# Performance work log

Hardware: AMD Instinct MI355X
Metric: run time of the kernel (lower is better)

## Reference

```python
import jax, jax.numpy as jnp
import numpy as np

DIM = 512
HEADS = 8
DH = DIM // HEADS          # 64
M = DIM // 2               # 256 landmarks
PINV_ITERS = 6
KERNEL = 33                # residual_conv_kernel (lucidrains default)
SCALE = DH ** -0.5
LN_EPS = 1e-5


def setup_inputs() -> dict:
    key = jax.random.key(0)
    ks = jax.random.split(key, 6)
    b, n = 4, 4096
    x = jax.random.normal(ks[0], (b, n, DIM), jnp.float32)
    ln_w = jnp.ones((DIM,), jnp.float32)
    ln_b = jnp.zeros((DIM,), jnp.float32)
    w_qkv = jax.random.normal(ks[1], (DIM, 3 * DIM), jnp.float32) / np.float32(np.sqrt(DIM))
    w_out = jax.random.normal(ks[2], (DIM, DIM), jnp.float32) / np.float32(np.sqrt(DIM))
    b_out = jnp.zeros((DIM,), jnp.float32)
    # depthwise Conv2d(heads, heads, (33,1), groups=heads, bias=False): OIHW = (8,1,33,1)
    conv_w = jax.random.normal(ks[3], (HEADS, 1, KERNEL, 1), jnp.float32) / np.float32(np.sqrt(KERNEL))
    # admin_torch.as_module(8): residual x*omega + f(x), omega learnable scalar init sqrt(8)
    omega = jnp.asarray(np.sqrt(8.0), jnp.float32)
    return dict(x=x, ln_w=ln_w, ln_b=ln_b, w_qkv=w_qkv, w_out=w_out,
                b_out=b_out, conv_w=conv_w, omega=omega)


def _layernorm(x, w, b):
    mu = x.mean(-1, keepdims=True)
    var = x.var(-1, keepdims=True)
    return (x - mu) * jax.lax.rsqrt(var + LN_EPS) * w + b


def _moore_penrose_pinv(x, iters):
    # Newton-Schulz iteration, exactly as lucidrains nystrom-attention
    abs_x = jnp.abs(x)
    col = abs_x.sum(-1)
    row = abs_x.sum(-2)
    z = jnp.swapaxes(x, -1, -2) / (jnp.max(col) * jnp.max(row))
    I = jnp.eye(x.shape[-1], dtype=x.dtype)
    for _ in range(iters):
        xz = x @ z
        z = 0.25 * z @ (13. * I - xz @ (15. * I - xz @ (7. * I - xz)))
    return z


def reference(x, ln_w, ln_b, w_qkv, w_out, b_out, conv_w, omega):
    b, n, _ = x.shape
    nx = _layernorm(x, ln_w, ln_b)
    qkv = nx @ w_qkv                                # [b, n, 3*dim]
    q, k, v = jnp.split(qkv, 3, axis=-1)
    to_heads = lambda t: t.reshape(b, n, HEADS, DH).transpose(0, 2, 1, 3)  # bhnd
    q = to_heads(q) * SCALE
    k = to_heads(k)
    v = to_heads(v)
    l = n // M                                      # tokens per landmark group
    q_l = q.reshape(b, HEADS, M, l, DH).mean(3)     # [b,h,m,d]
    k_l = k.reshape(b, HEADS, M, l, DH).mean(3)
    sim1 = jnp.einsum('bhid,bhjd->bhij', q, k_l)    # [b,h,n,m]
    sim2 = jnp.einsum('bhid,bhjd->bhij', q_l, k_l)  # [b,h,m,m]
    sim3 = jnp.einsum('bhid,bhjd->bhij', q_l, k)    # [b,h,m,n]
    a1 = jax.nn.softmax(sim1, -1)
    a2 = jax.nn.softmax(sim2, -1)
    a3 = jax.nn.softmax(sim3, -1)
    a2_inv = _moore_penrose_pinv(a2, PINV_ITERS)
    out = (a1 @ a2_inv) @ (a3 @ v)                  # [b,h,n,d]
    # residual depthwise conv along the sequence dim of v
    res = jax.lax.conv_general_dilated(
        v, conv_w, window_strides=(1, 1),
        padding=((KERNEL // 2, KERNEL // 2), (0, 0)),
        dimension_numbers=('NCHW', 'OIHW', 'NCHW'),
        feature_group_count=HEADS)
    out = out + res
    out = out.transpose(0, 2, 1, 3).reshape(b, n, HEADS * DH)
    out = out @ w_out + b_out                       # to_out (dropout is eval no-op)
    return x * omega + out                          # admin residual
```

## Files before the change

### kernel.cpp

```cpp
#include <hip/hip_runtime.h>
#include <math.h>

#define B_    4
#define N_    4096
#define DIM_  512
#define H_    8
#define DH_   64
#define M_    256
#define LGRP  16
#define BH_   (B_*H_)
#define SCALE_ 0.125f
#define LN_EPS_ 1e-5f

#define SZ_QKVH (B_*H_*N_*DH_)
#define SZ_LM   (BH_*M_*DH_)
#define SZ_MM   (BH_*M_*M_)

typedef unsigned short ushort_t;
typedef __attribute__((ext_vector_type(8))) short bfrag8;
typedef __attribute__((ext_vector_type(4))) float fvec4;

__device__ __forceinline__ ushort_t f2b(float f) {
    unsigned u = __float_as_uint(f);
    unsigned r = (u + 0x7fffu + ((u >> 16) & 1u)) >> 16;
    return (ushort_t)r;
}
__device__ __forceinline__ float b2f(ushort_t s) {
    return __uint_as_float(((unsigned)s) << 16);
}

__global__ __launch_bounds__(256) void ln_kernel(const float* __restrict__ x,
                                                 const float* __restrict__ w,
                                                 const float* __restrict__ bb,
                                                 ushort_t* __restrict__ nxb) {
    int row = blockIdx.x;
    int t = threadIdx.x;
    const float* xr = x + (size_t)row * DIM_;
    float v0 = xr[t], v1 = xr[t + 256];
    float s = v0 + v1, sq = v0 * v0 + v1 * v1;
    __shared__ float ls[4], lq[4];
    for (int off = 32; off > 0; off >>= 1) {
        s  += __shfl_down(s, off);
        sq += __shfl_down(sq, off);
    }
    int wid = t >> 6, lid = t & 63;
    if (lid == 0) { ls[wid] = s; lq[wid] = sq; }
    __syncthreads();
    if (t == 0) {
        float S = 0, Q = 0;
        for (int i = 0; i < 4; i++) { S += ls[i]; Q += lq[i]; }
        ls[0] = S; lq[0] = Q;
    }
    __syncthreads();
    float mean = ls[0] * (1.f / DIM_);
    float var  = lq[0] * (1.f / DIM_) - mean * mean;
    float rs = rsqrtf(var + LN_EPS_);
    ushort_t* o = nxb + (size_t)row * DIM_;
    o[t]       = f2b((v0 - mean) * rs * w[t]       + bb[t]);
    o[t + 256] = f2b((v1 - mean) * rs * w[t + 256] + bb[t + 256]);
}

__global__ __launch_bounds__(256) void tcast(const float* __restrict__ in,
                                             ushort_t* __restrict__ outT,
                                             int R, int C) {
    __shared__ float tile[32][33];
    int c0 = blockIdx.x * 32, r0 = blockIdx.y * 32;
    int t = threadIdx.x;
    #pragma unroll
    for (int u = 0; u < 4; u++) {
        int lin = t + 256 * u;
        int r = lin >> 5, c = lin & 31;
        tile[r][c] = in[(size_t)(r0 + r) * C + c0 + c];
    }
    __syncthreads();
    #pragma unroll
    for (int u = 0; u < 4; u++) {
        int lin = t + 256 * u;
        int cc = lin >> 5, rr = lin & 31;
        outT[(size_t)(c0 + cc) * R + r0 + rr] = f2b(tile[rr][cc]);
    }
}

template<int EPI>
__global__ __launch_bounds__(256) void gemm_bt128(const ushort_t* __restrict__ A,
                                                  const ushort_t* __restrict__ BT,
                                                  ushort_t* __restrict__ qb,
                                                  ushort_t* __restrict__ kb,
                                                  ushort_t* __restrict__ vb,
                                                  const float* __restrict__ x,
                                                  const float* __restrict__ bo,
                                                  const float* __restrict__ omega,
                                                  float* __restrict__ out) {
    const int K = 512;
    __shared__ __align__(16) ushort_t smem[2 * 128 * 72];
    ushort_t (*As)[72] = (ushort_t(*)[72])smem;
    ushort_t (*Bs)[72] = (ushort_t(*)[72])(smem + 128 * 72);
    int t = threadIdx.x;
    int lin = blockIdx.x + blockIdx.y * gridDim.x;
    int nwg = gridDim.x * gridDim.y;
    int wg  = (lin & 7) * (nwg >> 3) + (lin >> 3);
    int n0 = (wg % gridDim.x) * 128, m0 = (wg / gridDim.x) * 128;
    int w = t >> 6, lane = t & 63;
    int wr = (w >> 1) * 64, wc = (w & 1) * 64;
    int l15 = lane & 15, quad = lane >> 4, kq = quad * 8;
    fvec4 acc[4][4] = {};
    int rbase = t >> 3, c8 = (t & 7) * 8;

    for (int kc = 0; kc < K; kc += 64) {
        #pragma unroll
        for (int u = 0; u < 4; u++) {
            int rr = rbase + 32 * u;
            const ushort_t* ga;
            if (EPI == 0) {
                ga = A + (size_t)(m0 + rr) * K + kc + c8;
            } else {
                int grow = m0 + rr; int b_ = grow >> 12, nn = grow & 4095;
                int col = kc + c8; int hd = col >> 6, dd = col & 63;
                ga = A + (((size_t)(b_ * H_ + hd) * N_ + nn) << 6) + dd;
            }
            *(float4*)&As[rr][c8] = *(const float4*)ga;
            *(float4*)&Bs[rr][c8] = *(const float4*)(BT + (size_t)(n0 + rr) * K + kc + c8);
        }
        __syncthreads();
        #pragma unroll
        for (int ks = 0; ks < 64; ks += 32) {
            bfrag8 a[4], b[4];
            #pragma unroll
            for (int r = 0; r < 4; r++) a[r] = *(bfrag8*)&As[wr + r * 16 + l15][ks + kq];
            #pragma unroll
            for (int c = 0; c < 4; c++) b[c] = *(bfrag8*)&Bs[wc + c * 16 + l15][ks + kq];
            #pragma unroll
            for (int r = 0; r < 4; r++)
                #pragma unroll
                for (int c = 0; c < 4; c++)
                    acc[r][c] = __builtin_amdgcn_mfma_f32_16x16x32_bf16(a[r], b[c], acc[r][c], 0, 0, 0);
        }
        __syncthreads();
    }

    if (EPI == 0) {
        int sec = n0 >> 9;
        float mul = (sec == 0) ? SCALE_ : 1.0f;
        ushort_t (*Ct)[132] = (ushort_t(*)[132])smem;
        #pragma unroll
        for (int r = 0; r < 4; r++) {
            #pragma unroll
            for (int reg = 0; reg < 4; reg++) {
                int lr = wr + r * 16 + quad * 4 + reg;
                #pragma unroll
                for (int c = 0; c < 4; c++) {
                    int lc = wc + c * 16 + l15;
                    Ct[lr][lc] = f2b(acc[r][c][reg] * mul);
                }
            }
        }
        __syncthreads();
        int row = t & 127, half = t >> 7;
        int grow = m0 + row; int b_ = grow >> 12, nn = grow & 4095;
        int head = ((n0 & 511) >> 6) + half;
        ushort_t* dstbuf = (sec == 0) ? qb : ((sec == 1) ? kb : vb);
        ushort_t* dp = dstbuf + (((size_t)(b_ * H_ + head) * N_ + nn) << 6);
        #pragma unroll
        for (int i = 0; i < 8; i++)
            *(uint4*)(dp + i * 8) = *(uint4*)&Ct[row][half * 64 + i * 8];
    } else {
        float om = omega[0];
        #pragma unroll
        for (int r = 0; r < 4; r++) {
            #pragma unroll
            for (int reg = 0; reg < 4; reg++) {
                int grow = m0 + wr + r * 16 + quad * 4 + reg;
                #pragma unroll
                for (int c = 0; c < 4; c++) {
                    int gcol = n0 + wc + c * 16 + l15;
                    size_t o = (size_t)grow * DIM_ + gcol;
                    out[o] = om * x[o] + bo[gcol] + acc[r][c][reg];
                }
            }
        }
    }
}

__global__ __launch_bounds__(256) void landmark_kernel(const ushort_t* __restrict__ q,
                                                       const ushort_t* __restrict__ k,
                                                       ushort_t* __restrict__ ql,
                                                       ushort_t* __restrict__ kl) {
    int idx = blockIdx.x * 256 + threadIdx.x;
    const ushort_t* src = blockIdx.y ? k : q;
    ushort_t* dst = blockIdx.y ? kl : ql;
    int d8 = (idx & 7) * 8;
    int m = (idx >> 3) & 255;
    int bh = idx >> 11;
    const ushort_t* p = src + (((size_t)bh * N_) + m * LGRP) * DH_ + d8;
    float s[8] = {};
    #pragma unroll
    for (int j = 0; j < LGRP; j++) {
        union { uint4 u4; ushort_t sv[8]; } val;
        val.u4 = *(const uint4*)(p + (size_t)j * DH_);
        #pragma unroll
        for (int e = 0; e < 8; e++) s[e] += b2f(val.sv[e]);
    }
    union { uint4 u4; ushort_t sv[8]; } o;
    #pragma unroll
    for (int e = 0; e < 8; e++) o.sv[e] = f2b(s[e] * (1.f / LGRP));
    *(uint4*)(dst + ((size_t)bh * M_ + m) * DH_ + d8) = o.u4;
}

__global__ __launch_bounds__(256) void sim2_softmax(const ushort_t* __restrict__ ql,
                                                    const ushort_t* __restrict__ kl,
                                                    float* __restrict__ a2,
                                                    ushort_t* __restrict__ a2b) {
    int i = blockIdx.x, bh = blockIdx.y, j = threadIdx.x;
    __shared__ float qrow[64];
    __shared__ float red[256];
    if (j < 64) qrow[j] = b2f(ql[((size_t)bh * M_ + i) * DH_ + j]);
    __syncthreads();
    const ushort_t* kr = kl + ((size_t)bh * M_ + j) * DH_;
    float s = 0;
    #pragma unroll
    for (int d = 0; d < 64; d++) s += qrow[d] * b2f(kr[d]);
    red[j] = s; __syncthreads();
    for (int off = 128; off > 0; off >>= 1) {
        if (j < off) red[j] = fmaxf(red[j], red[j + off]);
        __syncthreads();
    }
    float mx = red[0]; __syncthreads();
    float p = __expf(s - mx);
    red[j] = p; __syncthreads();
    for (int off = 128; off > 0; off >>= 1) {
        if (j < off) red[j] += red[j + off];
        __syncthreads();
    }
    float res = p / red[0];
    size_t o = ((size_t)bh * M_ + i) * M_ + j;
    a2[o] = res;
    a2b[o] = f2b(res);
}

__global__ void zero2(unsigned* p) { if (threadIdx.x < 2) p[threadIdx.x] = 0u; }

__global__ __launch_bounds__(256) void colpart(const float* __restrict__ a2,
                                               float* __restrict__ cs2) {
    int bh = blockIdx.x, s = blockIdx.y, t = threadIdx.x;
    const float* A = a2 + ((size_t)bh << 16) + (size_t)s * 32 * M_;
    float cs = 0.f;
    #pragma unroll
    for (int i = 0; i < 32; i++) cs += A[(size_t)i * M_ + t];
    cs2[((size_t)s * BH_ + bh) * M_ + t] = cs;
}

__global__ __launch_bounds__(256) void colmax(const float* __restrict__ cs2, unsigned* red) {
    int bh = blockIdx.x, t = threadIdx.x;
    float v = 0.f;
    #pragma unroll
    for (int s = 0; s < 8; s++) v += cs2[((size_t)s * BH_ + bh) * M_ + t];
    __shared__ float lr[256];
    lr[t] = v; __syncthreads();
    for (int off = 128; off > 0; off >>= 1) {
        if (t < off) lr[t] = fmaxf(lr[t], lr[t + off]);
        __syncthreads();
    }
    if (t == 0) atomicMax(red, __float_as_uint(lr[0]));
}

__global__ __launch_bounds__(256) void pinv_init2(const float* __restrict__ a2,
                                                  const unsigned* __restrict__ red,
                                                  ushort_t* __restrict__ zA,
                                                  ushort_t* __restrict__ zAT) {
    __shared__ float tile[32][33];
    int bt = blockIdx.z; int j0 = blockIdx.x * 32, i0 = blockIdx.y * 32;
    float invd = 1.f / __uint_as_float(red[0]);
    const float* Ab = a2 + ((size_t)bt << 16);
    size_t bo = (size_t)bt << 16;
    int t = threadIdx.x;
    #pragma unroll
    for (int u = 0; u < 4; u++) {
        int lin = t + 256 * u; int r = lin >> 5, c = lin & 31;
        float vv = Ab[(size_t)(i0 + r) * M_ + j0 + c] * invd;
        tile[r][c] = vv;
        zAT[bo + (size_t)(i0 + r) * M_ + j0 + c] = f2b(vv);
    }
    __syncthreads();
    #pragma unroll
    for (int u = 0; u < 4; u++) {
        int lin = t + 256 * u; int cc = lin >> 5, rr = lin & 31;
        zA[bo + (size_t)(j0 + cc) * M_ + i0 + rr] = f2b(tile[rr][cc]);
    }
}

__global__ __launch_bounds__(256) void gemm_pinv(const ushort_t* __restrict__ A,
                                                 const ushort_t* __restrict__ BT,
                                                 ushort_t* __restrict__ outN,
                                                 ushort_t* __restrict__ outT,
                                                 ushort_t* __restrict__ outT1,
                                                 float* __restrict__ outF,
                                                 float coefI, float scale) {
    __shared__ __align__(16) ushort_t As[64][72];
    __shared__ __align__(16) ushort_t Bs[64][72];
    int t = threadIdx.x; int bt = blockIdx.z;
    const ushort_t* Ab = A + ((size_t)bt << 16);
    const ushort_t* Bb = BT + ((size_t)bt << 16);
    int n0 = blockIdx.x * 64, m0 = blockIdx.y * 64;
    int w = t >> 6, lane = t & 63;
    int wr = (w >> 1) * 32, wc = (w & 1) * 32;
    int l15 = lane & 15, quad = lane >> 4, kq = quad * 8;
    fvec4 acc[2][2] = {};
    int rbase = t >> 3, c8 = (t & 7) * 8;

    for (int kc = 0; kc < M_; kc += 64) {
        #pragma unroll
        for (int u = 0; u < 2; u++) {
            int rr = rbase + 32 * u;
            *(float4*)&As[rr][c8] = *(const float4*)(Ab + (size_t)(m0 + rr) * M_ + kc + c8);
            *(float4*)&Bs[rr][c8] = *(const float4*)(Bb + (size_t)(n0 + rr) * M_ + kc + c8);
        }
        __syncthreads();
        #pragma unroll
        for (int ks = 0; ks < 64; ks += 32) {
            bfrag8 a[2], b[2];
            #pragma unroll
            for (int r = 0; r < 2; r++) a[r] = *(bfrag8*)&As[wr + r * 16 + l15][ks + kq];
            #pragma unroll
            for (int c = 0; c < 2; c++) b[c] = *(bfrag8*)&Bs[wc + c * 16 + l15][ks + kq];
            #pragma unroll
            for (int r = 0; r < 2; r++)
                #pragma unroll
                for (int c = 0; c < 2; c++)
                    acc[r][c] = __builtin_amdgcn_mfma_f32_16x16x32_bf16(a[r], b[c], acc[r][c], 0, 0, 0);
        }
        __syncthreads();
    }

    size_t bto = (size_t)bt << 16;
    if (outN || outF) {
        #pragma unroll
        for (int r = 0; r < 2; r++) {
            #pragma unroll
            for (int reg = 0; reg < 4; reg++) {
                int grow = m0 + wr + r * 16 + quad * 4 + reg;
                #pragma unroll
                for (int c = 0; c < 2; c++) {
                    int gcol = n0 + wc + c * 16 + l15;
                    float cv = scale * acc[r][c][reg] + (grow == gcol ? coefI : 0.f);
                    if (outN) outN[bto + (size_t)grow * M_ + gcol] = f2b(cv);
                    if (outF) outF[bto + (size_t)grow * M_ + gcol] = cv;
                }
            }
        }
    }
    if (outT || outT1) {
        ushort_t (*Ct)[65] = (ushort_t(*)[65])&As[0][0];
        #pragma unroll
        for (int r = 0; r < 2; r++) {
            #pragma unroll
            for (int reg = 0; reg < 4; reg++) {
                int lr = wr + r * 16 + quad * 4 + reg;
                #pragma unroll
                for (int c = 0; c < 2; c++) {
                    int lc = wc + c * 16 + l15;
                    float cv = scale * acc[r][c][reg] + ((m0 + lr) == (n0 + lc) ? coefI : 0.f);
                    Ct[lr][lc] = f2b(cv);
                }
            }
        }
        __syncthreads();
        int j = t & 63, quarter = t >> 6, i0 = quarter * 16;
        #pragma unroll
        for (int vq = 0; vq < 2; vq++) {
            union { uint4 u4; ushort_t s[8]; } o1, o2;
            #pragma unroll
            for (int e = 0; e < 8; e++) {
                int il = i0 + vq * 8 + e;
                ushort_t bv = Ct[il][j];
                o1.s[e] = bv;
                o2.s[e] = f2b(((m0 + il) == (n0 + j) ? 7.f : 0.f) - b2f(bv));
            }
            size_t dst = bto + (size_t)(n0 + j) * M_ + m0 + i0 + vq * 8;
            if (outT)  *(uint4*)&outT[dst]  = o1.u4;
            if (outT1) *(uint4*)&outT1[dst] = o2.u4;
        }
    }
}

template<int NCH, int TRANSV>
__global__ __launch_bounds__(256) void flash_mfma(const ushort_t* __restrict__ Q,
                                                  const ushort_t* __restrict__ K,
                                                  const ushort_t* __restrict__ V,
                                                  ushort_t* __restrict__ Obf,
                                                  float* __restrict__ Opart,
                                                  float* __restrict__ lout,
                                                  int nq, int nk) {
    int bh = blockIdx.y;
    int nqt = nq >> 6;
    int qt = blockIdx.x % nqt;
    int ch = blockIdx.x / nqt;
    int q0 = qt * 64;
    int chunk = nk / NCH;
    int j0 = ch * chunk, j1 = j0 + chunk;

    __shared__ __align__(16) ushort_t qs[64][72];
    __shared__ __align__(16) ushort_t ks[64][72];
    __shared__ __align__(16) ushort_t vts[64][72];
    __shared__ __align__(16) ushort_t pb[64][72];

    int t = threadIdx.x;
    int w = t >> 6, lane = t & 63;
    int l15 = lane & 15, quad = lane >> 4, kq = quad * 8;
    int wrow = w * 16;

    const ushort_t* Qb = Q + ((size_t)bh * nq + q0) * DH_;
    #pragma unroll
    for (int u = 0; u < 2; u++) {
        int lin = t + 256 * u;
        int r = lin >> 3, cc = (lin & 7) * 8;
        *(uint4*)&qs[r][cc] = *(const uint4*)(Qb + r * DH_ + cc);
    }

    fvec4 Oacc[4];
    #pragma unroll
    for (int nt = 0; nt < 4; nt++)
        #pragma unroll
        for (int reg = 0; reg < 4; reg++) Oacc[nt][reg] = 0.f;
    float l_[4] = {0.f, 0.f, 0.f, 0.f};

    const ushort_t* VTbase = V + (size_t)bh * DH_ * nk;
    for (int j = j0; j < j1; j += 64) {
        const ushort_t* Kb = K + ((size_t)bh * nk + j) * DH_;
        const ushort_t* Vb = V + ((size_t)bh * nk + j) * DH_;
        #pragma unroll
        for (int u = 0; u < 2; u++) {
            int lin = t + 256 * u;
            int r = lin >> 3, cc = (lin & 7) * 8;
            *(uint4*)&ks[r][cc] = *(const uint4*)(Kb + r * DH_ + cc);
            if (TRANSV == 0) {
                *(uint4*)&vts[r][cc] = *(const uint4*)(VTbase + (size_t)r * nk + j + cc);
            } else {
                union { uint4 u4; ushort_t s[8]; } vv;
                vv.u4 = *(const uint4*)(Vb + r * DH_ + cc);
                #pragma unroll
                for (int m = 0; m < 8; m++) vts[cc + m][r] = vv.s[m];
            }
        }
        __syncthreads();

        fvec4 S[4];
        #pragma unroll
        for (int ct = 0; ct < 4; ct++)
            #pragma unroll
            for (int reg = 0; reg < 4; reg++) S[ct][reg] = 0.f;
        bfrag8 aq0 = *(bfrag8*)&qs[wrow + l15][kq];
        bfrag8 aq1 = *(bfrag8*)&qs[wrow + l15][32 + kq];
        #pragma unroll
        for (int ct = 0; ct < 4; ct++) {
            bfrag8 b0 = *(bfrag8*)&ks[ct * 16 + l15][kq];
            bfrag8 b1 = *(bfrag8*)&ks[ct * 16 + l15][32 + kq];
            S[ct] = __builtin_amdgcn_mfma_f32_16x16x32_bf16(aq0, b0, S[ct], 0, 0, 0);
            S[ct] = __builtin_amdgcn_mfma_f32_16x16x32_bf16(aq1, b1, S[ct], 0, 0, 0);
        }

        float ps[4] = {0.f, 0.f, 0.f, 0.f};
        #pragma unroll
        for (int ct = 0; ct < 4; ct++) {
            #pragma unroll
            for (int reg = 0; reg < 4; reg++) {
                float pv = __expf(S[ct][reg]);
                ps[reg] += pv;
                pb[wrow + quad * 4 + reg][ct * 16 + l15] = f2b(pv);
            }
        }
        #pragma unroll
        for (int reg = 0; reg < 4; reg++) {
            float s = ps[reg];
            s += __shfl_xor(s, 1);
            s += __shfl_xor(s, 2);
            s += __shfl_xor(s, 4);
            s += __shfl_xor(s, 8);
            l_[reg] += s;
        }

        bfrag8 ap0 = *(bfrag8*)&pb[wrow + l15][kq];
        bfrag8 ap1 = *(bfrag8*)&pb[wrow + l15][32 + kq];
        #pragma unroll
        for (int nt = 0; nt < 4; nt++) {
            bfrag8 b0 = *(bfrag8*)&vts[nt * 16 + l15][kq];
            bfrag8 b1 = *(bfrag8*)&vts[nt * 16 + l15][32 + kq];
            Oacc[nt] = __builtin_amdgcn_mfma_f32_16x16x32_bf16(ap0, b0, Oacc[nt], 0, 0, 0);
            Oacc[nt] = __builtin_amdgcn_mfma_f32_16x16x32_bf16(ap1, b1, Oacc[nt], 0, 0, 0);
        }
        __syncthreads();
    }

    if (NCH == 1) {
        #pragma unroll
        for (int reg = 0; reg < 4; reg++) {
            float inv = 1.f / l_[reg];
            #pragma unroll
            for (int nt = 0; nt < 4; nt++)
                qs[wrow + quad * 4 + reg][nt * 16 + l15] = f2b(Oacc[nt][reg] * inv);
        }
        __syncthreads();
        ushort_t* Ob = Obf + ((size_t)bh * nq + q0) * DH_;
        #pragma unroll
        for (int u = 0; u < 2; u++) {
            int lin = t + 256 * u;
            int r = lin >> 3, i = (lin & 7) * 8;
            *(uint4*)(Ob + (size_t)r * DH_ + i) = *(uint4*)&qs[r][i];
        }
    } else {
        size_t rows_per_ch = (size_t)BH_ * nq;
        #pragma unroll
        for (int reg = 0; reg < 4; reg++) {
            size_t rowg = (size_t)bh * nq + q0 + wrow + quad * 4 + reg;
            #pragma unroll
            for (int nt = 0; nt < 4; nt++)
                Opart[((size_t)ch * rows_per_ch + rowg) * DH_ + nt * 16 + l15] = Oacc[nt][reg];
            if (l15 == 0)
                lout[(size_t)ch * rows_per_ch + rowg] = l_[reg];
        }
    }
}

__global__ __launch_bounds__(256) void flash_combine(const float* __restrict__ apart,
                                                     const float* __restrict__ lpart,
                                                     ushort_t* __restrict__ a3vb) {
    int idx = blockIdx.x * 256 + threadIdx.x;
    int d = idx & 63; int row = idx >> 6;
    const int R = BH_ * M_;
    float l = lpart[row] + lpart[row + R] + lpart[row + 2 * R] + lpart[row + 3 * R];
    size_t e = (size_t)row * DH_ + d;
    const size_t CH = (size_t)R * DH_;
    float o = apart[e] + apart[e + CH] + apart[e + 2 * CH] + apart[e + 3 * CH];
    a3vb[e] = f2b(o / l);
}

__global__ __launch_bounds__(256) void wm_mfma(const ushort_t* __restrict__ Z,
                                               const ushort_t* __restrict__ A3V,
                                               ushort_t* __restrict__ WmT) {
    __shared__ __align__(16) ushort_t As[64][72];
    __shared__ __align__(16) ushort_t Bs[64][72];
    int bh = blockIdx.y;
    int i0 = blockIdx.x * 64;
    const ushort_t* Zb = Z + ((size_t)bh << 16);
    const ushort_t* Ab = A3V + ((size_t)bh << 14);
    int t = threadIdx.x;
    int w = t >> 6, lane = t & 63;
    int wr = (w >> 1) * 32, wc = (w & 1) * 32;
    int l15 = lane & 15, quad = lane >> 4, kq = quad * 8;
    fvec4 acc[2][2] = {};
    int rbase = t >> 3, c8 = (t & 7) * 8;

    for (int kc = 0; kc < M_; kc += 64) {
        #pragma unroll
        for (int u = 0; u < 2; u++) {
            int rr = rbase + 32 * u;
            *(float4*)&Bs[rr][c8] = *(const float4*)(Zb + (size_t)(i0 + rr) * M_ + kc + c8);
            union { uint4 u4; ushort_t s[8]; } av;
            av.u4 = *(const uint4*)(Ab + (size_t)(kc + rr) * DH_ + c8);
            #pragma unroll
            for (int m = 0; m < 8; m++) As[c8 + m][rr] = av.s[m];
        }
        __syncthreads();
        #pragma unroll
        for (int ks = 0; ks < 64; ks += 32) {
            bfrag8 a[2], b[2];
            #pragma unroll
            for (int r = 0; r < 2; r++) a[r] = *(bfrag8*)&As[wr + r * 16 + l15][ks + kq];
            #pragma unroll
            for (int c = 0; c < 2; c++) b[c] = *(bfrag8*)&Bs[wc + c * 16 + l15][ks + kq];
            #pragma unroll
            for (int r = 0; r < 2; r++)
                #pragma unroll
                for (int c = 0; c < 2; c++)
                    acc[r][c] = __builtin_amdgcn_mfma_f32_16x16x32_bf16(a[r], b[c], acc[r][c], 0, 0, 0);
        }
        __syncthreads();
    }
    #pragma unroll
    for (int r = 0; r < 2; r++) {
        #pragma unroll
        for (int reg = 0; reg < 4; reg++) {
            int drow = wr + r * 16 + quad * 4 + reg;
            ushort_t* dp = WmT + ((size_t)bh * DH_ + drow) * M_;
            #pragma unroll
            for (int c = 0; c < 2; c++)
                dp[i0 + wc + c * 16 + l15] = f2b(acc[r][c][reg]);
        }
    }
}

__global__ __launch_bounds__(256) void conv_kernel(const ushort_t* __restrict__ V,
                                                   const float* __restrict__ cw,
                                                   const ushort_t* __restrict__ ctxb,
                                                   ushort_t* __restrict__ outb) {
    int bh = blockIdx.y;
    int h = bh & 7;
    int i0 = blockIdx.x * 64;
    __shared__ float vb[96][64];
    __shared__ float wloc[33];
    int t = threadIdx.x;
    if (t < 33) wloc[t] = cw[h * 33 + t];
    #pragma unroll
    for (int u = 0; u < 3; u++) {
        int lin = t + 256 * u;
        int r = lin >> 3, cc = (lin & 7) * 8;
        int gi = i0 - 16 + r;
        union { uint4 u4; ushort_t s[8]; } val;
        if (gi >= 0 && gi < N_)
            val.u4 = *(const uint4*)(V + ((size_t)bh * N_ + gi) * DH_ + cc);
        else
            val.u4 = make_uint4(0, 0, 0, 0);
        #pragma unroll
        for (int m = 0; m < 8; m++) vb[r][cc + m] = b2f(val.s[m]);
    }
    __syncthreads();
    int d = t & 63, rb = t >> 6;
    for (int u = 0; u < 16; u++) {
        int r = rb * 16 + u;
        float s = 0.f;
        #pragma unroll
        for (int kk = 0; kk < 33; kk++) s += wloc[kk] * vb[r + kk][d];
        size_t o = ((size_t)bh * N_ + i0 + r) * DH_ + d;
        outb[o] = f2b(b2f(ctxb[o]) + s);
    }
}

extern "C" void kernel_launch(void* const* d_in, const int* in_sizes, int n_in,
                              void* d_out, int out_size, void* d_ws, size_t ws_size,
                              hipStream_t stream) {
    const float* x      = (const float*)d_in[0];
    const float* ln_w   = (const float*)d_in[1];
    const float* ln_b   = (const float*)d_in[2];
    const float* w_qkv  = (const float*)d_in[3];
    const float* w_out  = (const float*)d_in[4];
    const float* b_out  = (const float*)d_in[5];
    const float* conv_w = (const float*)d_in[6];
    const float* omega  = (const float*)d_in[7];
    float* out = (float*)d_out;

    float* fp = (float*)d_ws;
    float* a2    = fp;              fp += SZ_MM;
    float* apart = fp;              fp += SZ_QKVH / 4;
    float* lpart = fp;              fp += 4 * BH_ * M_;
    float* cs2   = fp;              fp += 8 * BH_ * M_;
    ushort_t* us = (ushort_t*)fp;
    ushort_t* wqkvT = us;           us += DIM_ * 3 * DIM_;
    ushort_t* woT   = us;           us += DIM_ * DIM_;
    ushort_t* a2b   = us;           us += SZ_MM;
    ushort_t* zA    = us;           us += SZ_MM;
    ushort_t* zAT   = us;           us += SZ_MM;
    ushort_t* zB    = us;           us += SZ_MM;
    ushort_t* zBT   = us;           us += SZ_MM;
    ushort_t* qb    = us;           us += SZ_QKVH;
    ushort_t* kb    = us;           us += SZ_QKVH;
    ushort_t* vb    = us;           us += SZ_QKVH;
    ushort_t* ctxb  = us;           us += SZ_QKVH;
    ushort_t* outhb = us;           us += SZ_QKVH;
    ushort_t* ql    = us;           us += SZ_LM;
    ushort_t* kl    = us;           us += SZ_LM;
    ushort_t* WmT   = us;           us += SZ_LM;
    ushort_t* a3vb  = us;           us += SZ_LM;
    unsigned* red   = (unsigned*)us;
    ushort_t* nxb = outhb;
    ushort_t* xz  = ctxb;
    ushort_t* t1T = xz  + SZ_MM;
    ushort_t* t2T = t1T + SZ_MM;
    ushort_t* t3T = t2T + SZ_MM;

    ln_kernel<<<B_ * N_, 256, 0, stream>>>(x, ln_w, ln_b, nxb);
    tcast<<<dim3(48, 16), 256, 0, stream>>>(w_qkv, wqkvT, DIM_, 3 * DIM_);
    tcast<<<dim3(16, 16), 256, 0, stream>>>(w_out, woT, DIM_, DIM_);
    gemm_bt128<0><<<dim3(12, 128), 256, 0, stream>>>(nxb, wqkvT, qb, kb, vb,
                                                     nullptr, nullptr, nullptr, nullptr);
    landmark_kernel<<<dim3(256, 2), 256, 0, stream>>>(qb, kb, ql, kl);
    sim2_softmax<<<dim3(M_, BH_), 256, 0, stream>>>(ql, kl, a2, a2b);
    zero2<<<1, 64, 0, stream>>>(red);
    colpart<<<dim3(BH_, 8), 256, 0, stream>>>(a2, cs2);
    colmax<<<BH_, 256, 0, stream>>>(cs2, red);
    pinv_init2<<<dim3(8, 8, 32), 256, 0, stream>>>(a2, red, zA, zAT);

    ushort_t* za = zA;  ushort_t* zaT = zAT;
    ushort_t* zb = zB;  ushort_t* zbT = zBT;
    for (int it = 0; it < 6; it++) {
        gemm_pinv<<<dim3(4, 4, BH_), 256, 0, stream>>>(a2b, zaT, xz, nullptr, t1T, nullptr, 0.f, 1.f);
        gemm_pinv<<<dim3(4, 4, BH_), 256, 0, stream>>>(xz, t1T, nullptr, t2T, nullptr, nullptr, 15.f, -1.f);
        gemm_pinv<<<dim3(4, 4, BH_), 256, 0, stream>>>(xz, t2T, nullptr, t3T, nullptr, nullptr, 13.f, -1.f);
        gemm_pinv<<<dim3(4, 4, BH_), 256, 0, stream>>>(za, t3T, zb, (it < 5) ? zbT : nullptr,
                                                       nullptr, nullptr, 0.f, 0.25f);
        ushort_t* tp;
        tp = za; za = zb; zb = tp;
        tp = zaT; zaT = zbT; zbT = tp;
    }

    flash_mfma<4, 1><<<dim3(16, BH_), 256, 0, stream>>>(ql, kb, vb, nullptr, apart, lpart, M_, N_);
    flash_combine<<<(BH_ * M_ * DH_) / 256, 256, 0, stream>>>(apart, lpart, a3vb);
    wm_mfma<<<dim3(4, BH_), 256, 0, stream>>>(za, a3vb, WmT);
    flash_mfma<1, 0><<<dim3(64, BH_), 256, 0, stream>>>(qb, kl, WmT, ctxb, nullptr, nullptr, N_, M_);
    conv_kernel<<<dim3(N_ / 64, BH_), 256, 0, stream>>>(vb, conv_w, ctxb, outhb);
    gemm_bt128<1><<<dim3(4, 128), 256, 0, stream>>>(outhb, woT, nullptr, nullptr, nullptr,
                                                    x, b_out, omega, out);
}
```

Measured before the change: 523.7 us.

## Double-buffer GEMM tiles via direct global-to-LDS loads and prefetch attention K/V

The QKV/output GEMM and the pinv GEMM now stage tiles with global_load_lds straight into LDS, double-buffering so the next k-tile loads while MFMAs run on the current one. The pinv GEMM also gets a swizzled workgroup-to-tile mapping for locality. The attention kernel prefetches the next K/V block into registers before the current compute. The aim is to hide global load latency. In exchange the LDS row padding is removed, which may cause bank conflicts, and correct synchronisation of asynchronous LDS writes is a risk.

```diff
diff --git a/kernel.cpp b/kernel.cpp
--- a/kernel.cpp
+++ b/kernel.cpp
@@ -27,6 +27,12 @@
 }
 __device__ __forceinline__ float b2f(ushort_t s) {
     return __uint_as_float(((unsigned)s) << 16);
+}
+
+__device__ __forceinline__ void gload16(const ushort_t* g, ushort_t* l) {
+    __builtin_amdgcn_global_load_lds(
+        (const __attribute__((address_space(1))) void*)g,
+        (__attribute__((address_space(3))) void*)l, 16, 0, 0);
 }
 
 __global__ __launch_bounds__(256) void ln_kernel(const float* __restrict__ x,
@@ -92,9 +98,7 @@
                                                   const float* __restrict__ omega,
                                                   float* __restrict__ out) {
     const int K = 512;
-    __shared__ __align__(16) ushort_t smem[2 * 128 * 72];
-    ushort_t (*As)[72] = (ushort_t(*)[72])smem;
-    ushort_t (*Bs)[72] = (ushort_t(*)[72])(smem + 128 * 72);
+    __shared__ __align__(16) ushort_t smem[4 * 128 * 64];
     int t = threadIdx.x;
     int lin = blockIdx.x + blockIdx.y * gridDim.x;
     int nwg = gridDim.x * gridDim.y;
@@ -103,32 +107,42 @@
     int w = t >> 6, lane = t & 63;
     int wr = (w >> 1) * 64, wc = (w & 1) * 64;
     int l15 = lane & 15, quad = lane >> 4, kq = quad * 8;
+    int lrow = lane >> 3, lc8 = (lane & 7) * 8;
     fvec4 acc[4][4] = {};
-    int rbase = t >> 3, c8 = (t & 7) * 8;
-
-    for (int kc = 0; kc < K; kc += 64) {
+
+    auto stage = [&](int buf, int kc) {
+        ushort_t* Ad = smem + buf * 16384;
+        ushort_t* Bd = Ad + 8192;
         #pragma unroll
         for (int u = 0; u < 4; u++) {
-            int rr = rbase + 32 * u;
+            int r0 = (w << 5) + (u << 3);
+            int row = r0 + lrow;
             const ushort_t* ga;
             if (EPI == 0) {
-                ga = A + (size_t)(m0 + rr) * K + kc + c8;
+                ga = A + (size_t)(m0 + row) * K + kc + lc8;
             } else {
-                int grow = m0 + rr; int b_ = grow >> 12, nn = grow & 4095;
-                int col = kc + c8; int hd = col >> 6, dd = col & 63;
-                ga = A + (((size_t)(b_ * H_ + hd) * N_ + nn) << 6) + dd;
+                int grow = m0 + row; int b_ = grow >> 12, nn = grow & 4095;
+                ga = A + (((size_t)(b_ * H_ + (kc >> 6)) * N_ + nn) << 6) + lc8;
             }
-            *(float4*)&As[rr][c8] = *(const float4*)ga;
-            *(float4*)&Bs[rr][c8] = *(const float4*)(BT + (size_t)(n0 + rr) * K + kc + c8);
-        }
-        __syncthreads();
+            gload16(ga, Ad + r0 * 64);
+            gload16(BT + (size_t)(n0 + row) * K + kc + lc8, Bd + r0 * 64);
+        }
+    };
+
+    stage(0, 0);
+    __syncthreads();
+    int cur = 0;
+    for (int kt = 0; kt < 8; ++kt) {
+        if (kt < 7) stage(cur ^ 1, (kt + 1) * 64);
+        const ushort_t* As = smem + cur * 16384;
+        const ushort_t* Bs = As + 8192;
         #pragma unroll
         for (int ks = 0; ks < 64; ks += 32) {
             bfrag8 a[4], b[4];
             #pragma unroll
-            for (int r = 0; r < 4; r++) a[r] = *(bfrag8*)&As[wr + r * 16 + l15][ks + kq];
-            #pragma unroll
-            for (int c = 0; c < 4; c++) b[c] = *(bfrag8*)&Bs[wc + c * 16 + l15][ks + kq];
+            for (int r = 0; r < 4; r++) a[r] = *(bfrag8*)(As + (wr + r * 16 + l15) * 64 + ks + kq);
+            #pragma unroll
+            for (int c = 0; c < 4; c++) b[c] = *(bfrag8*)(Bs + (wc + c * 16 + l15) * 64 + ks + kq);
             #pragma unroll
             for (int r = 0; r < 4; r++)
                 #pragma unroll
@@ -136,6 +150,7 @@
                     acc[r][c] = __builtin_amdgcn_mfma_f32_16x16x32_bf16(a[r], b[c], acc[r][c], 0, 0, 0);
         }
         __syncthreads();
+        cur ^= 1;
     }
 
     if (EPI == 0) {
@@ -295,33 +310,46 @@
                                                  ushort_t* __restrict__ outT1,
                                                  float* __restrict__ outF,
                                                  float coefI, float scale) {
-    __shared__ __align__(16) ushort_t As[64][72];
-    __shared__ __align__(16) ushort_t Bs[64][72];
-    int t = threadIdx.x; int bt = blockIdx.z;
+    __shared__ __align__(16) ushort_t smem[2 * 8192];
+    int t = threadIdx.x;
+    int lin = blockIdx.x + (blockIdx.y << 2) + (blockIdx.z << 4);
+    int wg  = (lin & 7) * 64 + (lin >> 3);
+    int n0 = (wg & 3) * 64, m0 = ((wg >> 2) & 3) * 64;
+    int bt = wg >> 4;
     const ushort_t* Ab = A + ((size_t)bt << 16);
     const ushort_t* Bb = BT + ((size_t)bt << 16);
-    int n0 = blockIdx.x * 64, m0 = blockIdx.y * 64;
     int w = t >> 6, lane = t & 63;
     int wr = (w >> 1) * 32, wc = (w & 1) * 32;
     int l15 = lane & 15, quad = lane >> 4, kq = quad * 8;
+    int lrow = lane >> 3, lc8 = (lane & 7) * 8;
     fvec4 acc[2][2] = {};
-    int rbase = t >> 3, c8 = (t & 7) * 8;
-
-    for (int kc = 0; kc < M_; kc += 64) {
+
+    auto stage = [&](int buf, int kc) {
+        ushort_t* Ad = smem + buf * 8192;
+        ushort_t* Bd = Ad + 4096;
         #pragma unroll
         for (int u = 0; u < 2; u++) {
-            int rr = rbase + 32 * u;
-            *(float4*)&As[rr][c8] = *(const float4*)(Ab + (size_t)(m0 + rr) * M_ + kc + c8);
-            *(float4*)&Bs[rr][c8] = *(const float4*)(Bb + (size_t)(n0 + rr) * M_ + kc + c8);
-        }
-        __syncthreads();
+            int r0 = (w << 4) + (u << 3);
+            int row = r0 + lrow;
+            gload16(Ab + (size_t)(m0 + row) * M_ + kc + lc8, Ad + r0 * 64);
+            gload16(Bb + (size_t)(n0 + row) * M_ + kc + lc8, Bd + r0 * 64);
+        }
+    };
+
+    stage(0, 0);
+    __syncthreads();
+    int cur = 0;
+    for (int kt = 0; kt < 4; ++kt) {
+        if (kt < 3) stage(cur ^ 1, (kt + 1) * 64);
+        const ushort_t* As = smem + cur * 8192;
+        const ushort_t* Bs = As + 4096;
         #pragma unroll
         for (int ks = 0; ks < 64; ks += 32) {
             bfrag8 a[2], b[2];
             #pragma unroll
-            for (int r = 0; r < 2; r++) a[r] = *(bfrag8*)&As[wr + r * 16 + l15][ks + kq];
-            #pragma unroll
-            for (int c = 0; c < 2; c++) b[c] = *(bfrag8*)&Bs[wc + c * 16 + l15][ks + kq];
+            for (int r = 0; r < 2; r++) a[r] = *(bfrag8*)(As + (wr + r * 16 + l15) * 64 + ks + kq);
+            #pragma unroll
+            for (int c = 0; c < 2; c++) b[c] = *(bfrag8*)(Bs + (wc + c * 16 + l15) * 64 + ks + kq);
             #pragma unroll
             for (int r = 0; r < 2; r++)
                 #pragma unroll
@@ -329,6 +357,7 @@
                     acc[r][c] = __builtin_amdgcn_mfma_f32_16x16x32_bf16(a[r], b[c], acc[r][c], 0, 0, 0);
         }
         __syncthreads();
+        cur ^= 1;
     }
 
     size_t bto = (size_t)bt << 16;
@@ -349,7 +378,7 @@
         }
     }
     if (outT || outT1) {
-        ushort_t (*Ct)[65] = (ushort_t(*)[65])&As[0][0];
+        ushort_t (*Ct)[65] = (ushort_t(*)[65])&smem[0];
         #pragma unroll
         for (int r = 0; r < 2; r++) {
             #pragma unroll
@@ -424,24 +453,43 @@
     float l_[4] = {0.f, 0.f, 0.f, 0.f};
 
     const ushort_t* VTbase = V + (size_t)bh * DH_ * nk;
-    for (int j = j0; j < j1; j += 64) {
+
+    uint4 kreg[2], vreg[2];
+    auto loadkv = [&](int j) {
         const ushort_t* Kb = K + ((size_t)bh * nk + j) * DH_;
-        const ushort_t* Vb = V + ((size_t)bh * nk + j) * DH_;
         #pragma unroll
         for (int u = 0; u < 2; u++) {
             int lin = t + 256 * u;
             int r = lin >> 3, cc = (lin & 7) * 8;
-            *(uint4*)&ks[r][cc] = *(const uint4*)(Kb + r * DH_ + cc);
+            kreg[u] = *(const uint4*)(Kb + r * DH_ + cc);
+            if (TRANSV == 0)
+                vreg[u] = *(const uint4*)(VTbase + (size_t)r * nk + j + cc);
+            else
+                vreg[u] = *(const uint4*)(V + ((size_t)(bh * nk + j + r)) * DH_ + cc);
+        }
+    };
+    auto writekv = [&]() {
+        #pragma unroll
+        for (int u = 0; u < 2; u++) {
+            int lin = t + 256 * u;
+            int r = lin >> 3, cc = (lin & 7) * 8;
+            *(uint4*)&ks[r][cc] = kreg[u];
             if (TRANSV == 0) {
-                *(uint4*)&vts[r][cc] = *(const uint4*)(VTbase + (size_t)r * nk + j + cc);
+                *(uint4*)&vts[r][cc] = vreg[u];
             } else {
                 union { uint4 u4; ushort_t s[8]; } vv;
-                vv.u4 = *(const uint4*)(Vb + r * DH_ + cc);
+                vv.u4 = vreg[u];
                 #pragma unroll
                 for (int m = 0; m < 8; m++) vts[cc + m][r] = vv.s[m];
             }
         }
-        __syncthreads();
+    };
+
+    loadkv(j0);
+    for (int j = j0; j < j1; j += 64) {
+        writekv();
+        __syncthreads();
+        if (j + 64 < j1) loadkv(j + 64);
 
         fvec4 S[4];
         #pragma unroll
```

Result: faster. 500.8 us (-4.4%).
